# Optimization experiments

Measured on AMD Instinct MI355X. Metric: run time of the kernel, lower is better.

The kernel has to match this reference:

```python
import jax, jax.numpy as jnp
import numpy as np

INPUT_DIM = 1024
NUM_OUTPUTS = 1024
BIT_SIZE = 256


def setup_inputs() -> dict:
    key = jax.random.key(0)
    k1, k2 = jax.random.split(key)
    # x: binary input bits, shape (input_dim, bit_size)
    x = jax.random.randint(k1, (INPUT_DIM, BIT_SIZE), 0, 2).astype(jnp.int32)
    # kernel: per-(input, output) Bernoulli probabilities in [0, 1)
    kernel = jax.random.uniform(k2, (INPUT_DIM, NUM_OUTPUTS), dtype=jnp.float32)
    return {"x": x, "kernel": kernel}


def reference(x, kernel):
    # Sample per-weight Bernoulli bit vectors: w[i, n, b] ~ Bernoulli(kernel[i, n])
    # (fused equivalent of the original nested-loop np.random.binomial calls)
    rng = jax.random.key(42)
    u = jax.random.uniform(rng, kernel.shape + (BIT_SIZE,), dtype=kernel.dtype)
    w = u < kernel[:, :, None]  # bool (input_dim, num_outputs, bit_size)

    # Original loop: temp = (x & w[:, n]).sum(axis=0); y[n] = (temp > 0)
    # == OR-reduction over input_dim of the bitwise AND.
    xb = x.astype(bool)  # (input_dim, bit_size)
    y = jnp.any(xb[:, None, :] & w, axis=0)  # (num_outputs, bit_size)
    return y.astype(jnp.float32)
```

## Files before the change

### kernel.cpp

```cpp
#include <hip/hip_runtime.h>


#define INPUT_DIM 1024
#define NUM_OUTPUTS 1024
#define BIT_SIZE 256

__device__ __forceinline__ uint32_t rotl32(uint32_t v, int r) {
    return (v << r) | (v >> (32 - r));
}

__device__ __forceinline__ void threefry2x32(uint32_t k0, uint32_t k1,
                                             uint32_t& x0, uint32_t& x1) {
    const uint32_t ks0 = k0;
    const uint32_t ks1 = k1;
    const uint32_t ks2 = k0 ^ k1 ^ 0x1BD11BDAu;
    x0 += ks0;
    x1 += ks1;
#define TF_ROUND(r) { x0 += x1; x1 = rotl32(x1, (r)); x1 ^= x0; }
    TF_ROUND(13) TF_ROUND(15) TF_ROUND(26) TF_ROUND(6)
    x0 += ks1; x1 += ks2 + 1u;
    TF_ROUND(17) TF_ROUND(29) TF_ROUND(16) TF_ROUND(24)
    x0 += ks2; x1 += ks0 + 2u;
    TF_ROUND(13) TF_ROUND(15) TF_ROUND(26) TF_ROUND(6)
    x0 += ks0; x1 += ks1 + 3u;
    TF_ROUND(17) TF_ROUND(29) TF_ROUND(16) TF_ROUND(24)
    x0 += ks1; x1 += ks2 + 4u;
    TF_ROUND(13) TF_ROUND(15) TF_ROUND(26) TF_ROUND(6)
    x0 += ks2; x1 += ks0 + 5u;
#undef TF_ROUND
}

__global__ __launch_bounds__(256) void BitLayer_25391846654323_kernel(
        const int* __restrict__ x,
        const float* __restrict__ kern,
        float* __restrict__ out) {
    const int b = threadIdx.x;
    const int n = blockIdx.x;
    const uint32_t base = ((uint32_t)n << 8) | (uint32_t)b;

    float result = 0.0f;
    for (int i = 0; i < INPUT_DIM; ++i) {
        if (x[(i << 8) + b] != 0) {
            const float p = kern[(i << 10) + n];
            uint32_t c0 = (((uint32_t)(i & 511)) << 18) | base;
            uint32_t c1 = c0 + (1u << 27);
            threefry2x32(0u, 42u, c0, c1);
            const uint32_t bits = (i < 512) ? c0 : c1;
            const float u = (float)(bits >> 9) * 0x1p-23f;
            if (u < p) { result = 1.0f; break; }
        }
    }
    out[(n << 8) + b] = result;
}

extern "C" void kernel_launch(void* const* d_in, const int* in_sizes, int n_in,
                              void* d_out, int out_size, void* d_ws, size_t ws_size,
                              hipStream_t stream) {
    const int* x = (const int*)d_in[0];
    const float* kern = (const float*)d_in[1];
    float* out = (float*)d_out;

    BitLayer_25391846654323_kernel<<<NUM_OUTPUTS, BIT_SIZE, 0, stream>>>(x, kern, out);
}
```

Before: 72.81 us.

## Pack x into bitmasks and map threads over outputs for uniform sparse iteration

Adds a pre-pass that packs the binary x matrix into 32-bit masks per bit position. The main kernel now gives each block one bit column and lets threads span outputs, so every lane in a wavefront visits the same set of nonzero inputs. Kern loads become coalesced across n, and the wavefront exits early once all lanes have hit. This is meant to remove divergence, where lanes with different x bits serialized the threefry work, and the uncoalesced strided kern reads. It costs an extra kernel launch and relies on workspace memory.

Result: faster. 64.70 us (-11.1%).

```diff
diff --git a/kernel.cpp b/kernel.cpp
--- a/kernel.cpp
+++ b/kernel.cpp
@@ -30,27 +30,47 @@
 #undef TF_ROUND
 }
 
+__global__ __launch_bounds__(256) void pack_x_kernel(const int* __restrict__ x,
+                                                     uint32_t* __restrict__ xm) {
+    const int b = threadIdx.x;
+    const int w = blockIdx.x;
+    uint32_t m = 0;
+#pragma unroll
+    for (int j = 0; j < 32; ++j) {
+        m |= (x[(((w << 5) + j) << 8) + b] != 0 ? 1u : 0u) << j;
+    }
+    xm[(w << 8) + b] = m;
+}
+
 __global__ __launch_bounds__(256) void BitLayer_25391846654323_kernel(
-        const int* __restrict__ x,
+        const uint32_t* __restrict__ xm,
         const float* __restrict__ kern,
         float* __restrict__ out) {
-    const int b = threadIdx.x;
-    const int n = blockIdx.x;
-    const uint32_t base = ((uint32_t)n << 8) | (uint32_t)b;
+    const int b = blockIdx.x >> 2;
+    const int n = ((blockIdx.x & 3) << 8) + threadIdx.x;
+    uint32_t done = 0;
 
-    float result = 0.0f;
-    for (int i = 0; i < INPUT_DIM; ++i) {
-        if (x[(i << 8) + b] != 0) {
+    for (int w = 0; w < 32; ++w) {
+        uint32_t m = xm[(w << 8) + b];
+        while (m) {
+            const int j = __builtin_ctz(m);
+            m &= m - 1;
+            const int i = (w << 5) + j;
             const float p = kern[(i << 10) + n];
-            uint32_t c0 = (((uint32_t)(i & 511)) << 18) | base;
-            uint32_t c1 = c0 + (1u << 27);
-            threefry2x32(0u, 42u, c0, c1);
-            const uint32_t bits = (i < 512) ? c0 : c1;
-            const float u = (float)(bits >> 9) * 0x1p-23f;
-            if (u < p) { result = 1.0f; break; }
+            if (!done) {
+                uint32_t c0 = (((uint32_t)(i & 511)) << 18) |
+                              ((uint32_t)n << 8) | (uint32_t)b;
+                uint32_t c1 = c0 + (1u << 27);
+                threefry2x32(0u, 42u, c0, c1);
+                const uint32_t bits = (i < 512) ? c0 : c1;
+                const float u = (float)(bits >> 9) * 0x1p-23f;
+                if (u < p) done = 1u;
+            }
+            if (__all(done != 0)) goto finished;
         }
     }
-    out[(n << 8) + b] = result;
+finished:
+    out[((uint32_t)n << 8) + (uint32_t)b] = done ? 1.0f : 0.0f;
 }
 
 extern "C" void kernel_launch(void* const* d_in, const int* in_sizes, int n_in,
@@ -59,6 +79,8 @@
     const int* x = (const int*)d_in[0];
     const float* kern = (const float*)d_in[1];
     float* out = (float*)d_out;
+    uint32_t* xm = (uint32_t*)d_ws;
 
-    BitLayer_25391846654323_kernel<<<NUM_OUTPUTS, BIT_SIZE, 0, stream>>>(x, kern, out);
+    pack_x_kernel<<<32, 256, 0, stream>>>(x, xm);
+    BitLayer_25391846654323_kernel<<<NUM_OUTPUTS, 256, 0, stream>>>(xm, kern, out);
 }
```
